# Optimization experiments

Measured on AMD Instinct MI355X. Metric: run time of the kernel, lower is better.

## Reference

```python
import jax, jax.numpy as jnp
import numpy as np

P, H, B_SZ, L = 256, 128, 4, 4096

def setup_inputs() -> dict:
    key = jax.random.key(0)
    k1, k2, k3, k4, k5 = jax.random.split(key, 5)
    A_diag = jax.random.uniform(k1, (P,), dtype=jnp.float32)                 # [P], >=0 for stability
    B = jax.random.normal(k2, (P, H, 2), dtype=jnp.float32) / np.sqrt(H)     # [P,H,2] real+imag
    C = jax.random.normal(k3, (H, P, 2), dtype=jnp.float32) / np.sqrt(P)     # [H,P,2] real+imag
    input_sequence = jax.random.normal(k4, (B_SZ, L, H), dtype=jnp.float32)  # [B,L,H]
    step = jax.random.uniform(k5, (P,), dtype=jnp.float32, minval=0.01, maxval=1.0)  # [P], 0<dt<=1
    return {"A_diag": A_diag, "B": B, "C": C, "input_sequence": input_sequence, "step": step}

def reference(A_diag, B, C, input_sequence, step):
    # LinOSS-IM: implicit discretization of a diagonal oscillatory SSM.
    cdt = jnp.complex64
    B_c = (B[..., 0] + 1j * B[..., 1]).astype(cdt)           # [P,H]
    Bu = jnp.einsum('blh,ph->blp', input_sequence.astype(cdt), B_c)  # [B,L,P]
    A_c = A_diag.astype(cdt)
    s_c = step.astype(cdt)
    schur = 1.0 / (1.0 + s_c ** 2 * A_c)                      # (I + dt^2 A)^-1, diagonal
    M11 = 1.0 - s_c ** 2 * A_c * schur
    M12 = -s_c * A_c * schur
    M21 = s_c * schur
    M22 = schur
    F1 = M11 * (s_c * Bu)                                     # [B,L,P]
    F2 = M21 * (s_c * Bu)
    Bsz = input_sequence.shape[0]
    z0 = jnp.zeros((Bsz, A_diag.shape[0]), dtype=cdt)
    y0 = jnp.zeros((Bsz, A_diag.shape[0]), dtype=cdt)

    def step_fn(carry, f):
        z, y = carry
        f1, f2 = f
        z_new = M11 * z + M12 * y + f1
        y_new = M21 * z + M22 * y + f2
        return (z_new, y_new), y_new

    # scan over time axis L; move L to front
    (z_f, y_f), ys = jax.lax.scan(step_fn, (z0, y0),
                                  (jnp.swapaxes(F1, 0, 1), jnp.swapaxes(F2, 0, 1)))
    ys = jnp.swapaxes(ys, 0, 1)                               # [B,L,P]
    C_c = (C[..., 0] + 1j * C[..., 1]).astype(cdt)            # [H,P]
    out = jnp.einsum('blp,hp->blh', ys, C_c).real.astype(jnp.float32)  # [B,L,H]
    return out, (z_f, y_f)
```

## Files before the change

### kernel.cpp

```cpp
#include <hip/hip_runtime.h>
#include <cstddef>

#define P_DIM 256
#define H_DIM 128
#define B_SZ 4
#define L_SEQ 4096
#define PC 512
#define M_ROWS (B_SZ * L_SEQ)
#define CL 32
#define CLOG 5
#define NC (L_SEQ / CL)
#define OUT_BASE (B_SZ * L_SEQ * H_DIM)

#define USE_MFMA 1

typedef __attribute__((ext_vector_type(8))) short s8v;
typedef __attribute__((ext_vector_type(4))) float f32x4;

__device__ __forceinline__ unsigned short f2bf(float x) {
  unsigned u = __builtin_bit_cast(unsigned, x);
  unsigned r = (u + 0x7FFFu + ((u >> 16) & 1u)) >> 16;
  return (unsigned short)r;
}
__device__ __forceinline__ float bf2f(unsigned short h) {
  return __builtin_bit_cast(float, (unsigned)h << 16);
}
__device__ __forceinline__ void f2hl(float x, short& h, short& l) {
  unsigned short hb = f2bf(x);
  float hf = bf2f(hb);
  unsigned short lb = f2bf(x - hf);
  h = (short)hb; l = (short)lb;
}

__device__ __forceinline__ void make_M(const float* A_diag, const float* step, int p,
                                       float& M11, float& M12, float& M21, float& M22) {
  float Ad = A_diag[p], s = step[p];
  float sig = 1.0f / fmaf(s * s, Ad, 1.0f);
  M11 = 1.0f - s * s * Ad * sig;
  M12 = -s * Ad * sig;
  M21 = s * sig;
  M22 = sig;
}

#if USE_MFMA
__global__ __launch_bounds__(256) void prep_kernel(const float* __restrict__ Bin,
                                                   const float* __restrict__ Cin,
                                                   const float* __restrict__ step,
                                                   float* __restrict__ Bw,
                                                   short* __restrict__ CtH,
                                                   short* __restrict__ CtL) {
  int idx = blockIdx.x * 256 + threadIdx.x;
  {
    int kk = idx >> 7, h = idx & 127;
    int p = kk >> 1, c = kk & 1;
    Bw[idx] = step[p] * Bin[(p * H_DIM + h) * 2 + c];
  }
  {
    int j = idx & 7, lane = (idx >> 3) & 63, ks = (idx >> 9) & 15, nt = idx >> 13;
    int h = nt * 16 + (lane & 15);
    int k = ks * 32 + (lane >> 4) * 8 + j;
    float v = Cin[(size_t)h * PC + k] * ((k & 1) ? -1.0f : 1.0f);
    short hh, ll; f2hl(v, hh, ll);
    CtH[idx] = hh; CtL[idx] = ll;
  }
}

template<int KTOT, int LDC>
__global__ __launch_bounds__(256) void gemm_nt_mfma(const float* __restrict__ A,
                                                    const float* __restrict__ Bt,
                                                    float* __restrict__ Cout) {
  __shared__ short As_h[64][72], As_l[64][72];
  __shared__ short Bs_h[128][72], Bs_l[128][72];
  const int t = threadIdx.x;
  const int lane = t & 63;
  const int wid = t >> 6;
  const int wm = (wid & 1) * 32;
  const int wn = (wid >> 1) * 64;
  const int m0 = blockIdx.y * 64;
  const int n0 = blockIdx.x * 128;
  const int lr  = lane & 15;
  const int kb8 = (lane >> 4) * 8;
  const int ar = t >> 4;
  const int ac = (t & 15) * 4;

  f32x4 acc[2][4] = {};

  for (int ks = 0; ks < KTOT / 64; ++ks) {
    const int k0 = ks * 64;
    float4 av[4], bv[8];
#pragma unroll
    for (int j = 0; j < 4; ++j)
      av[j] = *(const float4*)&A[(size_t)(m0 + ar + 16 * j) * KTOT + k0 + ac];
#pragma unroll
    for (int j = 0; j < 8; ++j)
      bv[j] = *(const float4*)&Bt[(size_t)(n0 + ar + 16 * j) * KTOT + k0 + ac];
    __syncthreads();
#pragma unroll
    for (int j = 0; j < 4; ++j) {
      short4 h4, l4;
      f2hl(av[j].x, h4.x, l4.x); f2hl(av[j].y, h4.y, l4.y);
      f2hl(av[j].z, h4.z, l4.z); f2hl(av[j].w, h4.w, l4.w);
      *(short4*)&As_h[ar + 16 * j][ac] = h4;
      *(short4*)&As_l[ar + 16 * j][ac] = l4;
    }
#pragma unroll
    for (int j = 0; j < 8; ++j) {
      short4 h4, l4;
      f2hl(bv[j].x, h4.x, l4.x); f2hl(bv[j].y, h4.y, l4.y);
      f2hl(bv[j].z, h4.z, l4.z); f2hl(bv[j].w, h4.w, l4.w);
      *(short4*)&Bs_h[ar + 16 * j][ac] = h4;
      *(short4*)&Bs_l[ar + 16 * j][ac] = l4;
    }
    __syncthreads();
#pragma unroll
    for (int kb = 0; kb < 2; ++kb) {
      s8v ah[2], al[2], bh[4], bl[4];
#pragma unroll
      for (int ti = 0; ti < 2; ++ti) {
        ah[ti] = *(const s8v*)&As_h[wm + ti * 16 + lr][kb * 32 + kb8];
        al[ti] = *(const s8v*)&As_l[wm + ti * 16 + lr][kb * 32 + kb8];
      }
#pragma unroll
      for (int tj = 0; tj < 4; ++tj) {
        bh[tj] = *(const s8v*)&Bs_h[wn + tj * 16 + lr][kb * 32 + kb8];
        bl[tj] = *(const s8v*)&Bs_l[wn + tj * 16 + lr][kb * 32 + kb8];
      }
#pragma unroll
      for (int ti = 0; ti < 2; ++ti)
#pragma unroll
        for (int tj = 0; tj < 4; ++tj) {
          acc[ti][tj] = __builtin_amdgcn_mfma_f32_16x16x32_bf16(ah[ti], bh[tj], acc[ti][tj], 0, 0, 0);
          acc[ti][tj] = __builtin_amdgcn_mfma_f32_16x16x32_bf16(ah[ti], bl[tj], acc[ti][tj], 0, 0, 0);
          acc[ti][tj] = __builtin_amdgcn_mfma_f32_16x16x32_bf16(al[ti], bh[tj], acc[ti][tj], 0, 0, 0);
        }
    }
  }
  const int rb = (lane >> 4) * 4;
#pragma unroll
  for (int ti = 0; ti < 2; ++ti)
#pragma unroll
    for (int tj = 0; tj < 4; ++tj) {
      const int row = m0 + wm + ti * 16 + rb;
      const int col = n0 + wn + tj * 16 + lr;
#pragma unroll
      for (int r = 0; r < 4; ++r)
        Cout[(size_t)(row + r) * LDC + col] = acc[ti][tj][r];
    }
}

__global__ __launch_bounds__(512) void emit_gemm_kernel(const float* __restrict__ A_diag,
                                                        const float* __restrict__ step,
                                                        const float* __restrict__ carryIn,
                                                        const float* __restrict__ sBu,
                                                        const short* __restrict__ CtH,
                                                        const short* __restrict__ CtL,
                                                        float* __restrict__ outp) {
  __shared__ short ys_h[32][512];
  __shared__ short ys_l[32][512];
  const int t = threadIdx.x;
  const int b = blockIdx.y, ch = blockIdx.x;

  {
    const int p = t >> 1;
    float M11, M12, M21, M22;
    make_M(A_diag, step, p, M11, M12, M21, M22);
    size_t o = (((size_t)b * NC + ch) * PC + t) * 2;
    float z = carryIn[o], y = carryIn[o + 1];
    const float* fp = sBu + ((size_t)b * L_SEQ + (size_t)ch * CL) * PC + t;
#pragma unroll 8
    for (int i = 0; i < CL; ++i) {
      float f = fp[(size_t)i * PC];
      float zf = z + f;
      z = fmaf(M11, zf, M12 * y);
      y = fmaf(M21, zf, M22 * y);
      short hh, ll; f2hl(y, hh, ll);
      const int c = t ^ ((i & 7) << 3);
      ys_h[i][c] = hh;
      ys_l[i][c] = ll;
    }
  }
  __syncthreads();

  const int w = t >> 6, lane = t & 63;
  const int mt = w & 1;
  const int ntb = (w >> 1) * 2;
  const int lr = lane & 15, kb8 = (lane >> 4) * 8;
  const int mrow = mt * 16 + lr;
  const int msw = (mrow & 7) << 3;
  f32x4 acc[2] = {};
  for (int ks = 0; ks < 16; ++ks) {
    const int kc = (ks * 32 + kb8) ^ msw;
    s8v ah = *(const s8v*)&ys_h[mrow][kc];
    s8v al = *(const s8v*)&ys_l[mrow][kc];
#pragma unroll
    for (int q = 0; q < 2; ++q) {
      const int nt = ntb + q;
      size_t fo = (((size_t)nt * 16 + ks) * 64 + lane) * 8;
      s8v bh = *(const s8v*)&CtH[fo];
      s8v bl = *(const s8v*)&CtL[fo];
      acc[q] = __builtin_amdgcn_mfma_f32_16x16x32_bf16(ah, bh, acc[q], 0, 0, 0);
      acc[q] = __builtin_amdgcn_mfma_f32_16x16x32_bf16(al, bh, acc[q], 0, 0, 0);
      acc[q] = __builtin_amdgcn_mfma_f32_16x16x32_bf16(ah, bl, acc[q], 0, 0, 0);
    }
  }
  const int rb = (lane >> 4) * 4;
  const size_t rowbase = (size_t)b * L_SEQ + (size_t)ch * CL;
#pragma unroll
  for (int q = 0; q < 2; ++q) {
    const int col = (ntb + q) * 16 + lr;
#pragma unroll
    for (int r = 0; r < 4; ++r) {
      int m = mt * 16 + rb + r;
      outp[(rowbase + m) * H_DIM + col] = acc[q][r];
    }
  }
}
#else
__global__ __launch_bounds__(256) void prep_kernel_f32(const float* __restrict__ Bin,
                                                       const float* __restrict__ Cin,
                                                       const float* __restrict__ step,
                                                       float* __restrict__ Bw,
                                                       float* __restrict__ Ct) {
  int idx = blockIdx.x * 256 + threadIdx.x;
  int kk = idx >> 7, h = idx & 127;
  int p = kk >> 1, c = kk & 1;
  Bw[idx] = step[p] * Bin[(p * H_DIM + h) * 2 + c];
  float cv = Cin[(h * P_DIM + p) * 2 + c];
  Ct[idx] = (c == 0) ? cv : -cv;
}

__global__ __launch_bounds__(256) void gemm_nt_kernel(const float* __restrict__ A,
                                                      const float* __restrict__ Bm,
                                                      float* __restrict__ Cout) {
  __shared__ float As[16][132];
  __shared__ float Bs[16][132];
  const int t = threadIdx.x;
  const int m0 = blockIdx.y * 128;
  const int n0 = blockIdx.x * 128;
  const int tm0 = (t & 15) * 8;
  const int tn0 = (t >> 4) * 8;
  const int row = t >> 2;
  const int kq  = (t & 3) * 4;
  float acc[8][8] = {};
  for (int k0 = 0; k0 < 128; k0 += 16) {
    float4 a0 = *(const float4*)&A[(size_t)(m0 + row) * 128 + k0 + kq];
    float4 a1 = *(const float4*)&A[(size_t)(m0 + row + 64) * 128 + k0 + kq];
    float4 b0 = *(const float4*)&Bm[(size_t)(n0 + row) * 128 + k0 + kq];
    float4 b1 = *(const float4*)&Bm[(size_t)(n0 + row + 64) * 128 + k0 + kq];
    __syncthreads();
    As[kq + 0][row] = a0.x; As[kq + 1][row] = a0.y; As[kq + 2][row] = a0.z; As[kq + 3][row] = a0.w;
    As[kq + 0][row + 64] = a1.x; As[kq + 1][row + 64] = a1.y; As[kq + 2][row + 64] = a1.z; As[kq + 3][row + 64] = a1.w;
    Bs[kq + 0][row] = b0.x; Bs[kq + 1][row] = b0.y; Bs[kq + 2][row] = b0.z; Bs[kq + 3][row] = b0.w;
    Bs[kq + 0][row + 64] = b1.x; Bs[kq + 1][row + 64] = b1.y; Bs[kq + 2][row + 64] = b1.z; Bs[kq + 3][row + 64] = b1.w;
    __syncthreads();
#pragma unroll
    for (int k = 0; k < 16; ++k) {
      float4 a03 = *(const float4*)&As[k][tm0];
      float4 a47 = *(const float4*)&As[k][tm0 + 4];
      float4 b03 = *(const float4*)&Bs[k][tn0];
      float4 b47 = *(const float4*)&Bs[k][tn0 + 4];
      float av[8] = {a03.x, a03.y, a03.z, a03.w, a47.x, a47.y, a47.z, a47.w};
      float bv[8] = {b03.x, b03.y, b03.z, b03.w, b47.x, b47.y, b47.z, b47.w};
#pragma unroll
      for (int i = 0; i < 8; ++i)
#pragma unroll
        for (int j = 0; j < 8; ++j)
          acc[i][j] = fmaf(av[i], bv[j], acc[i][j]);
    }
  }
#pragma unroll
  for (int i = 0; i < 8; ++i) {
    float4 v0 = make_float4(acc[i][0], acc[i][1], acc[i][2], acc[i][3]);
    float4 v1 = make_float4(acc[i][4], acc[i][5], acc[i][6], acc[i][7]);
    *(float4*)&Cout[(size_t)(m0 + tm0 + i) * PC + n0 + tn0] = v0;
    *(float4*)&Cout[(size_t)(m0 + tm0 + i) * PC + n0 + tn0 + 4] = v1;
  }
}

__global__ __launch_bounds__(512) void scan_emit_kernel(const float* __restrict__ A_diag,
                                                        const float* __restrict__ step,
                                                        const float* __restrict__ carryIn,
                                                        float* __restrict__ sBu) {
  const int t = threadIdx.x;
  const int p = t >> 1;
  const int b = blockIdx.y;
  const int ch = blockIdx.x;
  float M11, M12, M21, M22;
  make_M(A_diag, step, p, M11, M12, M21, M22);
  size_t o = (((size_t)b * NC + ch) * PC + t) * 2;
  float z = carryIn[o], y = carryIn[o + 1];
  float* fp = sBu + ((size_t)b * L_SEQ + (size_t)ch * CL) * PC + t;
#pragma unroll 8
  for (int i = 0; i < CL; ++i) {
    float f = fp[(size_t)i * PC];
    float zf = z + f;
    z = fmaf(M11, zf, M12 * y);
    y = fmaf(M21, zf, M22 * y);
    fp[(size_t)i * PC] = y;
  }
}

__global__ __launch_bounds__(256) void gemm_nn_kernel(const float* __restrict__ A,
                                                      const float* __restrict__ Bm,
                                                      float* __restrict__ Cout) {
  __shared__ float As[16][132];
  __shared__ float Bs[16][68];
  const int t = threadIdx.x;
  const int m0 = blockIdx.y * 128;
  const int n0 = blockIdx.x * 64;
  const int tm0 = (t & 15) * 8;
  const int tn0 = (t >> 4) * 4;
  const int row = t >> 2;
  const int kq  = (t & 3) * 4;
  const int bk_row = t >> 4;
  const int bk_c4  = (t & 15) * 4;
  float acc[8][4] = {};
  for (int k0 = 0; k0 < 512; k0 += 16) {
    float4 a0 = *(const float4*)&A[(size_t)(m0 + row) * PC + k0 + kq];
    float4 a1 = *(const float4*)&A[(size_t)(m0 + row + 64) * PC + k0 + kq];
    float4 bv = *(const float4*)&Bm[(size_t)(k0 + bk_row) * H_DIM + n0 + bk_c4];
    __syncthreads();
    As[kq + 0][row] = a0.x; As[kq + 1][row] = a0.y; As[kq + 2][row] = a0.z; As[kq + 3][row] = a0.w;
    As[kq + 0][row + 64] = a1.x; As[kq + 1][row + 64] = a1.y; As[kq + 2][row + 64] = a1.z; As[kq + 3][row + 64] = a1.w;
    *(float4*)&Bs[bk_row][bk_c4] = bv;
    __syncthreads();
#pragma unroll
    for (int k = 0; k < 16; ++k) {
      float4 a03 = *(const float4*)&As[k][tm0];
      float4 a47 = *(const float4*)&As[k][tm0 + 4];
      float4 b03 = *(const float4*)&Bs[k][tn0];
      float av[8] = {a03.x, a03.y, a03.z, a03.w, a47.x, a47.y, a47.z, a47.w};
      float bv4[4] = {b03.x, b03.y, b03.z, b03.w};
#pragma unroll
      for (int i = 0; i < 8; ++i)
#pragma unroll
        for (int j = 0; j < 4; ++j)
          acc[i][j] = fmaf(av[i], bv4[j], acc[i][j]);
    }
  }
#pragma unroll
  for (int i = 0; i < 8; ++i) {
    float4 v = make_float4(acc[i][0], acc[i][1], acc[i][2], acc[i][3]);
    *(float4*)&Cout[(size_t)(m0 + tm0 + i) * H_DIM + n0 + tn0] = v;
  }
}
#endif

__global__ __launch_bounds__(512) void scan_local_kernel(const float* __restrict__ A_diag,
                                                         const float* __restrict__ step,
                                                         const float* __restrict__ sBu,
                                                         float* __restrict__ carries) {
  const int t = threadIdx.x;
  const int p = t >> 1;
  const int b = blockIdx.y;
  const int ch = blockIdx.x;
  float M11, M12, M21, M22;
  make_M(A_diag, step, p, M11, M12, M21, M22);
  const float* fp = sBu + ((size_t)b * L_SEQ + (size_t)ch * CL) * PC + t;
  float z = 0.f, y = 0.f;
#pragma unroll 8
  for (int i = 0; i < CL; ++i) {
    float f = fp[(size_t)i * PC];
    float zf = z + f;
    z = fmaf(M11, zf, M12 * y);
    y = fmaf(M21, zf, M22 * y);
  }
  size_t o = (((size_t)b * NC + ch) * PC + t) * 2;
  carries[o] = z; carries[o + 1] = y;
}

__global__ __launch_bounds__(512) void combine_kernel(const float* __restrict__ A_diag,
                                                      const float* __restrict__ step,
                                                      const float* __restrict__ carries,
                                                      float* __restrict__ carryIn,
                                                      float* __restrict__ outp,
                                                      int mode) {
  const int t = threadIdx.x;
  const int p = t >> 1;
  const int b = blockIdx.x;
  float M11, M12, M21, M22;
  make_M(A_diag, step, p, M11, M12, M21, M22);
  float X11 = M11, X12 = M12, X21 = M21, X22 = M22;
#pragma unroll
  for (int i = 0; i < CLOG; ++i) {
    float a = X11 * X11 + X12 * X21;
    float bb = X11 * X12 + X12 * X22;
    float cc = X21 * X11 + X22 * X21;
    float dd = X21 * X12 + X22 * X22;
    X11 = a; X12 = bb; X21 = cc; X22 = dd;
  }
  float z = 0.f, y = 0.f;
#pragma unroll 4
  for (int k = 0; k < NC; ++k) {
    size_t o = (((size_t)b * NC + k) * PC + t) * 2;
    carryIn[o] = z; carryIn[o + 1] = y;
    float sz = carries[o], sy = carries[o + 1];
    float zn = X11 * z + X12 * y + sz;
    float yn = X21 * z + X22 * y + sy;
    z = zn; y = yn;
  }
  const int c = t & 1;
  if (mode == 1) {
    if (c == 0) {
      outp[OUT_BASE + (size_t)b * 256 + p] = z;
      outp[OUT_BASE + 1024 + (size_t)b * 256 + p] = y;
    }
  } else if (mode == 2) {
    outp[OUT_BASE + (size_t)c * 1024 + (size_t)b * 256 + p] = z;
    outp[OUT_BASE + 2048 + (size_t)c * 1024 + (size_t)b * 256 + p] = y;
  } else {
    outp[OUT_BASE + (size_t)b * PC + t] = z;
    outp[OUT_BASE + 2048 + (size_t)b * PC + t] = y;
  }
}

extern "C" void kernel_launch(void* const* d_in, const int* in_sizes, int n_in,
                              void* d_out, int out_size, void* d_ws, size_t ws_size,
                              hipStream_t stream) {
  const float* A_diag = (const float*)d_in[0];
  const float* Bin    = (const float*)d_in[1];
  const float* Cin    = (const float*)d_in[2];
  const float* U      = (const float*)d_in[3];
  const float* step   = (const float*)d_in[4];
  float* outp = (float*)d_out;
  float* ws = (float*)d_ws;

  int mode;
  if (out_size == OUT_BASE + 2048) mode = 1;
  else if (out_size == OUT_BASE + 4096) mode = 2;
  else mode = 0;

  float* Bw      = ws;
  float* CtA     = Bw + 65536;
  float* sBu     = CtA + 65536;
  float* carries = sBu + 8388608;
  float* carryIn = carries + 524288;

#if USE_MFMA
  short* CtH = (short*)CtA;
  short* CtL = CtH + 65536;
  prep_kernel<<<256, 256, 0, stream>>>(Bin, Cin, step, Bw, CtH, CtL);
  gemm_nt_mfma<128, 512><<<dim3(4, 256), 256, 0, stream>>>(U, Bw, sBu);
  scan_local_kernel<<<dim3(NC, B_SZ), 512, 0, stream>>>(A_diag, step, sBu, carries);
  combine_kernel<<<B_SZ, 512, 0, stream>>>(A_diag, step, carries, carryIn, outp, mode);
  emit_gemm_kernel<<<dim3(NC, B_SZ), 512, 0, stream>>>(A_diag, step, carryIn, sBu,
                                                       CtH, CtL, outp);
#else
  prep_kernel_f32<<<256, 256, 0, stream>>>(Bin, Cin, step, Bw, CtA);
  gemm_nt_kernel<<<dim3(4, 128), 256, 0, stream>>>(U, Bw, sBu);
  scan_local_kernel<<<dim3(NC, B_SZ), 512, 0, stream>>>(A_diag, step, sBu, carries);
  combine_kernel<<<B_SZ, 512, 0, stream>>>(A_diag, step, carries, carryIn, outp, mode);
  scan_emit_kernel<<<dim3(NC, B_SZ), 512, 0, stream>>>(A_diag, step, carryIn, sBu);
  gemm_nn_kernel<<<dim3(2, 128), 256, 0, stream>>>(sBu, CtA, outp);
#endif
}
```

Baseline: 126.6 us.

## Fuse input GEMM, chunk scan, combine and emit into one cooperative kernel

Replaces the separate input GEMM, local scan, carry combine and emit+output-GEMM launches with a single cooperative kernel that uses grid-wide syncs between phases. Each block computes its 32-row slice of the projected input straight into shared memory with pre-split bf16 hi/lo weights, so the large intermediate sBu buffer is never written to or read back from global memory. The combine phase now runs in only the chunk-0 blocks while every other block waits at the grid barrier. This adds grid-sync overhead and a serialized combine, and keeps the old multi-kernel path as a fallback if the cooperative launch fails.

```diff
diff --git a/kernel.cpp b/kernel.cpp
--- a/kernel.cpp
+++ b/kernel.cpp
@@ -1,18 +1,18 @@
 #include <hip/hip_runtime.h>
+#include <hip/hip_cooperative_groups.h>
 #include <cstddef>
+
+namespace cg = cooperative_groups;
 
 #define P_DIM 256
 #define H_DIM 128
 #define B_SZ 4
 #define L_SEQ 4096
 #define PC 512
-#define M_ROWS (B_SZ * L_SEQ)
 #define CL 32
 #define CLOG 5
 #define NC (L_SEQ / CL)
 #define OUT_BASE (B_SZ * L_SEQ * H_DIM)
-
-#define USE_MFMA 1
 
 typedef __attribute__((ext_vector_type(8))) short s8v;
 typedef __attribute__((ext_vector_type(4))) float f32x4;
@@ -42,13 +42,14 @@
   M22 = sig;
 }
 
-#if USE_MFMA
 __global__ __launch_bounds__(256) void prep_kernel(const float* __restrict__ Bin,
                                                    const float* __restrict__ Cin,
                                                    const float* __restrict__ step,
                                                    float* __restrict__ Bw,
                                                    short* __restrict__ CtH,
-                                                   short* __restrict__ CtL) {
+                                                   short* __restrict__ CtL,
+                                                   short* __restrict__ BwH,
+                                                   short* __restrict__ BwL) {
   int idx = blockIdx.x * 256 + threadIdx.x;
   {
     int kk = idx >> 7, h = idx & 127;
@@ -62,6 +63,188 @@
     float v = Cin[(size_t)h * PC + k] * ((k & 1) ? -1.0f : 1.0f);
     short hh, ll; f2hl(v, hh, ll);
     CtH[idx] = hh; CtL[idx] = ll;
+  }
+  {
+    int j = idx & 7, lane = (idx >> 3) & 63, ks = (idx >> 9) & 3, nt = idx >> 11;
+    int n = nt * 16 + (lane & 15);
+    int k = ks * 32 + (lane >> 4) * 8 + j;
+    int p = n >> 1, c = n & 1;
+    float v = step[p] * Bin[(p * H_DIM + k) * 2 + c];
+    short hh, ll; f2hl(v, hh, ll);
+    BwH[idx] = hh; BwL[idx] = ll;
+  }
+}
+
+__global__ __launch_bounds__(512, 4) void mega_kernel(const float* __restrict__ A_diag,
+                                                      const float* __restrict__ step,
+                                                      const float* __restrict__ U,
+                                                      const short* __restrict__ BwH,
+                                                      const short* __restrict__ BwL,
+                                                      const short* __restrict__ CtH,
+                                                      const short* __restrict__ CtL,
+                                                      float* __restrict__ carries,
+                                                      float* __restrict__ carryIn,
+                                                      float* __restrict__ outp,
+                                                      int mode) {
+  __shared__ float Fs[32][512];
+  const int t = threadIdx.x;
+  const int ch = blockIdx.x;
+  const int b  = blockIdx.y;
+  const int lane = t & 63, w = t >> 6;
+  const int lr = lane & 15, kb8 = (lane >> 4) * 8, rb = (lane >> 4) * 4;
+
+  short* Ush = (short*)&Fs[0][0];
+  short* Usl = Ush + 32 * 136;
+  {
+    const int row = t >> 4, c8 = (t & 15) * 8;
+    const float* up = &U[((size_t)b * L_SEQ + (size_t)ch * CL + row) * H_DIM + c8];
+    float4 u0 = *(const float4*)up, u1 = *(const float4*)(up + 4);
+    s8v h8, l8; short hh, ll;
+    f2hl(u0.x, hh, ll); h8[0] = hh; l8[0] = ll;
+    f2hl(u0.y, hh, ll); h8[1] = hh; l8[1] = ll;
+    f2hl(u0.z, hh, ll); h8[2] = hh; l8[2] = ll;
+    f2hl(u0.w, hh, ll); h8[3] = hh; l8[3] = ll;
+    f2hl(u1.x, hh, ll); h8[4] = hh; l8[4] = ll;
+    f2hl(u1.y, hh, ll); h8[5] = hh; l8[5] = ll;
+    f2hl(u1.z, hh, ll); h8[6] = hh; l8[6] = ll;
+    f2hl(u1.w, hh, ll); h8[7] = hh; l8[7] = ll;
+    *(s8v*)&Ush[row * 136 + c8] = h8;
+    *(s8v*)&Usl[row * 136 + c8] = l8;
+  }
+  __syncthreads();
+
+  const int mt = w & 1;
+  const int ntbA = (w >> 1) * 8;
+  f32x4 accA[8] = {};
+#pragma unroll
+  for (int ks = 0; ks < 4; ++ks) {
+    s8v ah = *(const s8v*)&Ush[(mt * 16 + lr) * 136 + ks * 32 + kb8];
+    s8v al = *(const s8v*)&Usl[(mt * 16 + lr) * 136 + ks * 32 + kb8];
+#pragma unroll
+    for (int q = 0; q < 8; ++q) {
+      size_t fo = (((size_t)(ntbA + q) * 4 + ks) * 64 + lane) * 8;
+      s8v bh = *(const s8v*)&BwH[fo];
+      s8v bl = *(const s8v*)&BwL[fo];
+      accA[q] = __builtin_amdgcn_mfma_f32_16x16x32_bf16(ah, bh, accA[q], 0, 0, 0);
+      accA[q] = __builtin_amdgcn_mfma_f32_16x16x32_bf16(al, bh, accA[q], 0, 0, 0);
+      accA[q] = __builtin_amdgcn_mfma_f32_16x16x32_bf16(ah, bl, accA[q], 0, 0, 0);
+    }
+  }
+  __syncthreads();
+
+#pragma unroll
+  for (int q = 0; q < 8; ++q)
+#pragma unroll
+    for (int r = 0; r < 4; ++r) {
+      int row = mt * 16 + rb + r;
+      int col = (ntbA + q) * 16 + lr;
+      Fs[row][col ^ ((row & 7) << 3)] = accA[q][r];
+    }
+  __syncthreads();
+
+  float M11, M12, M21, M22;
+  make_M(A_diag, step, t >> 1, M11, M12, M21, M22);
+  {
+    float z = 0.f, y = 0.f;
+#pragma unroll 8
+    for (int i = 0; i < CL; ++i) {
+      float f = Fs[i][t ^ ((i & 7) << 3)];
+      float zf = z + f;
+      z = fmaf(M11, zf, M12 * y);
+      y = fmaf(M21, zf, M22 * y);
+    }
+    size_t o = (((size_t)b * NC + ch) * PC + t) * 2;
+    carries[o] = z; carries[o + 1] = y;
+  }
+  cg::this_grid().sync();
+
+  if (ch == 0) {
+    float X11 = M11, X12 = M12, X21 = M21, X22 = M22;
+#pragma unroll
+    for (int i = 0; i < CLOG; ++i) {
+      float a = X11 * X11 + X12 * X21;
+      float bb = X11 * X12 + X12 * X22;
+      float cc = X21 * X11 + X22 * X21;
+      float dd = X21 * X12 + X22 * X22;
+      X11 = a; X12 = bb; X21 = cc; X22 = dd;
+    }
+    float z = 0.f, y = 0.f;
+#pragma unroll 8
+    for (int k = 0; k < NC; ++k) {
+      size_t o = (((size_t)b * NC + k) * PC + t) * 2;
+      carryIn[o] = z; carryIn[o + 1] = y;
+      float sz = carries[o], sy = carries[o + 1];
+      float zn = X11 * z + X12 * y + sz;
+      float yn = X21 * z + X22 * y + sy;
+      z = zn; y = yn;
+    }
+    const int c = t & 1, p = t >> 1;
+    if (mode == 1) {
+      if (c == 0) {
+        outp[OUT_BASE + (size_t)b * 256 + p] = z;
+        outp[OUT_BASE + 1024 + (size_t)b * 256 + p] = y;
+      }
+    } else if (mode == 2) {
+      outp[OUT_BASE + (size_t)c * 1024 + (size_t)b * 256 + p] = z;
+      outp[OUT_BASE + 2048 + (size_t)c * 1024 + (size_t)b * 256 + p] = y;
+    } else {
+      outp[OUT_BASE + (size_t)b * PC + t] = z;
+      outp[OUT_BASE + 2048 + (size_t)b * PC + t] = y;
+    }
+  }
+  cg::this_grid().sync();
+
+  {
+    size_t o = (((size_t)b * NC + ch) * PC + t) * 2;
+    float z = carryIn[o], y = carryIn[o + 1];
+#pragma unroll 8
+    for (int i = 0; i < CL; ++i) {
+      const int cswz = t ^ ((i & 7) << 3);
+      float f = Fs[i][cswz];
+      float zf = z + f;
+      z = fmaf(M11, zf, M12 * y);
+      y = fmaf(M21, zf, M22 * y);
+      short hh, ll; f2hl(y, hh, ll);
+      unsigned u = ((unsigned)(unsigned short)hh << 16) | (unsigned)(unsigned short)ll;
+      Fs[i][cswz] = __builtin_bit_cast(float, u);
+    }
+  }
+  __syncthreads();
+
+  const int ntbC = (w >> 1) * 2;
+  const int mrow = mt * 16 + lr;
+  const int msw = (mrow & 7) << 3;
+  f32x4 accC[2] = {};
+  for (int ks = 0; ks < 16; ++ks) {
+    const unsigned* ap = (const unsigned*)&Fs[mrow][(ks * 32 + kb8) ^ msw];
+    uint4 w0 = *(const uint4*)ap;
+    uint4 w1 = *(const uint4*)(ap + 4);
+    s8v ah, al;
+    ah[0] = (short)(w0.x >> 16); al[0] = (short)(w0.x & 0xffff);
+    ah[1] = (short)(w0.y >> 16); al[1] = (short)(w0.y & 0xffff);
+    ah[2] = (short)(w0.z >> 16); al[2] = (short)(w0.z & 0xffff);
+    ah[3] = (short)(w0.w >> 16); al[3] = (short)(w0.w & 0xffff);
+    ah[4] = (short)(w1.x >> 16); al[4] = (short)(w1.x & 0xffff);
+    ah[5] = (short)(w1.y >> 16); al[5] = (short)(w1.y & 0xffff);
+    ah[6] = (short)(w1.z >> 16); al[6] = (short)(w1.z & 0xffff);
+    ah[7] = (short)(w1.w >> 16); al[7] = (short)(w1.w & 0xffff);
+#pragma unroll
+    for (int q = 0; q < 2; ++q) {
+      size_t fo = (((size_t)(ntbC + q) * 16 + ks) * 64 + lane) * 8;
+      s8v bh = *(const s8v*)&CtH[fo];
+      s8v bl = *(const s8v*)&CtL[fo];
+      accC[q] = __builtin_amdgcn_mfma_f32_16x16x32_bf16(ah, bh, accC[q], 0, 0, 0);
+      accC[q] = __builtin_amdgcn_mfma_f32_16x16x32_bf16(al, bh, accC[q], 0, 0, 0);
+      accC[q] = __builtin_amdgcn_mfma_f32_16x16x32_bf16(ah, bl, accC[q], 0, 0, 0);
+    }
+  }
+  const size_t rowbase = (size_t)b * L_SEQ + (size_t)ch * CL;
+#pragma unroll
+  for (int q = 0; q < 2; ++q) {
+    const int col = (ntbC + q) * 16 + lr;
+#pragma unroll
+    for (int r = 0; r < 4; ++r)
+      outp[(rowbase + mt * 16 + rb + r) * H_DIM + col] = accC[q][r];
   }
 }
 
@@ -82,9 +265,7 @@
   const int kb8 = (lane >> 4) * 8;
   const int ar = t >> 4;
   const int ac = (t & 15) * 4;
-
   f32x4 acc[2][4] = {};
-
   for (int ks = 0; ks < KTOT / 64; ++ks) {
     const int k0 = ks * 64;
     float4 av[4], bv[8];
@@ -146,6 +327,71 @@
       for (int r = 0; r < 4; ++r)
         Cout[(size_t)(row + r) * LDC + col] = acc[ti][tj][r];
     }
+}
+
+__global__ __launch_bounds__(512) void scan_local_kernel(const float* __restrict__ A_diag,
+                                                         const float* __restrict__ step,
+                                                         const float* __restrict__ sBu,
+                                                         float* __restrict__ carries) {
+  const int t = threadIdx.x;
+  const int b = blockIdx.y, ch = blockIdx.x;
+  float M11, M12, M21, M22;
+  make_M(A_diag, step, t >> 1, M11, M12, M21, M22);
+  const float* fp = sBu + ((size_t)b * L_SEQ + (size_t)ch * CL) * PC + t;
+  float z = 0.f, y = 0.f;
+#pragma unroll 8
+  for (int i = 0; i < CL; ++i) {
+    float f = fp[(size_t)i * PC];
+    float zf = z + f;
+    z = fmaf(M11, zf, M12 * y);
+    y = fmaf(M21, zf, M22 * y);
+  }
+  size_t o = (((size_t)b * NC + ch) * PC + t) * 2;
+  carries[o] = z; carries[o + 1] = y;
+}
+
+__global__ __launch_bounds__(512) void combine_kernel(const float* __restrict__ A_diag,
+                                                      const float* __restrict__ step,
+                                                      const float* __restrict__ carries,
+                                                      float* __restrict__ carryIn,
+                                                      float* __restrict__ outp,
+                                                      int mode) {
+  const int t = threadIdx.x;
+  const int b = blockIdx.x;
+  float M11, M12, M21, M22;
+  make_M(A_diag, step, t >> 1, M11, M12, M21, M22);
+  float X11 = M11, X12 = M12, X21 = M21, X22 = M22;
+#pragma unroll
+  for (int i = 0; i < CLOG; ++i) {
+    float a = X11 * X11 + X12 * X21;
+    float bb = X11 * X12 + X12 * X22;
+    float cc = X21 * X11 + X22 * X21;
+    float dd = X21 * X12 + X22 * X22;
+    X11 = a; X12 = bb; X21 = cc; X22 = dd;
+  }
+  float z = 0.f, y = 0.f;
+#pragma unroll 8
+  for (int k = 0; k < NC; ++k) {
+    size_t o = (((size_t)b * NC + k) * PC + t) * 2;
+    carryIn[o] = z; carryIn[o + 1] = y;
+    float sz = carries[o], sy = carries[o + 1];
+    float zn = X11 * z + X12 * y + sz;
+    float yn = X21 * z + X22 * y + sy;
+    z = zn; y = yn;
+  }
+  const int c = t & 1, p = t >> 1;
+  if (mode == 1) {
+    if (c == 0) {
+      outp[OUT_BASE + (size_t)b * 256 + p] = z;
+      outp[OUT_BASE + 1024 + (size_t)b * 256 + p] = y;
+    }
+  } else if (mode == 2) {
+    outp[OUT_BASE + (size_t)c * 1024 + (size_t)b * 256 + p] = z;
+    outp[OUT_BASE + 2048 + (size_t)c * 1024 + (size_t)b * 256 + p] = y;
+  } else {
+    outp[OUT_BASE + (size_t)b * PC + t] = z;
+    outp[OUT_BASE + 2048 + (size_t)b * PC + t] = y;
+  }
 }
 
 __global__ __launch_bounds__(512) void emit_gemm_kernel(const float* __restrict__ A_diag,
@@ -159,11 +405,9 @@
   __shared__ short ys_l[32][512];
   const int t = threadIdx.x;
   const int b = blockIdx.y, ch = blockIdx.x;
-
-  {
-    const int p = t >> 1;
+  {
     float M11, M12, M21, M22;
-    make_M(A_diag, step, p, M11, M12, M21, M22);
+    make_M(A_diag, step, t >> 1, M11, M12, M21, M22);
     size_t o = (((size_t)b * NC + ch) * PC + t) * 2;
     float z = carryIn[o], y = carryIn[o + 1];
     const float* fp = sBu + ((size_t)b * L_SEQ + (size_t)ch * CL) * PC + t;
@@ -180,7 +424,6 @@
     }
   }
   __syncthreads();
-
   const int w = t >> 6, lane = t & 63;
   const int mt = w & 1;
   const int ntb = (w >> 1) * 2;
@@ -194,8 +437,7 @@
     s8v al = *(const s8v*)&ys_l[mrow][kc];
 #pragma unroll
     for (int q = 0; q < 2; ++q) {
-      const int nt = ntb + q;
-      size_t fo = (((size_t)nt * 16 + ks) * 64 + lane) * 8;
+      size_t fo = (((size_t)(ntb + q) * 16 + ks) * 64 + lane) * 8;
       s8v bh = *(const s8v*)&CtH[fo];
       s8v bl = *(const s8v*)&CtL[fo];
       acc[q] = __builtin_amdgcn_mfma_f32_16x16x32_bf16(ah, bh, acc[q], 0, 0, 0);
@@ -209,208 +451,8 @@
   for (int q = 0; q < 2; ++q) {
     const int col = (ntb + q) * 16 + lr;
 #pragma unroll
-    for (int r = 0; r < 4; ++r) {
-      int m = mt * 16 + rb + r;
-      outp[(rowbase + m) * H_DIM + col] = acc[q][r];
-    }
-  }
-}
-#else
-__global__ __launch_bounds__(256) void prep_kernel_f32(const float* __restrict__ Bin,
-                                                       const float* __restrict__ Cin,
-                                                       const float* __restrict__ step,
-                                                       float* __restrict__ Bw,
-                                                       float* __restrict__ Ct) {
-  int idx = blockIdx.x * 256 + threadIdx.x;
-  int kk = idx >> 7, h = idx & 127;
-  int p = kk >> 1, c = kk & 1;
-  Bw[idx] = step[p] * Bin[(p * H_DIM + h) * 2 + c];
-  float cv = Cin[(h * P_DIM + p) * 2 + c];
-  Ct[idx] = (c == 0) ? cv : -cv;
-}
-
-__global__ __launch_bounds__(256) void gemm_nt_kernel(const float* __restrict__ A,
-                                                      const float* __restrict__ Bm,
-                                                      float* __restrict__ Cout) {
-  __shared__ float As[16][132];
-  __shared__ float Bs[16][132];
-  const int t = threadIdx.x;
-  const int m0 = blockIdx.y * 128;
-  const int n0 = blockIdx.x * 128;
-  const int tm0 = (t & 15) * 8;
-  const int tn0 = (t >> 4) * 8;
-  const int row = t >> 2;
-  const int kq  = (t & 3) * 4;
-  float acc[8][8] = {};
-  for (int k0 = 0; k0 < 128; k0 += 16) {
-    float4 a0 = *(const float4*)&A[(size_t)(m0 + row) * 128 + k0 + kq];
-    float4 a1 = *(const float4*)&A[(size_t)(m0 + row + 64) * 128 + k0 + kq];
-    float4 b0 = *(const float4*)&Bm[(size_t)(n0 + row) * 128 + k0 + kq];
-    float4 b1 = *(const float4*)&Bm[(size_t)(n0 + row + 64) * 128 + k0 + kq];
-    __syncthreads();
-    As[kq + 0][row] = a0.x; As[kq + 1][row] = a0.y; As[kq + 2][row] = a0.z; As[kq + 3][row] = a0.w;
-    As[kq + 0][row + 64] = a1.x; As[kq + 1][row + 64] = a1.y; As[kq + 2][row + 64] = a1.z; As[kq + 3][row + 64] = a1.w;
-    Bs[kq + 0][row] = b0.x; Bs[kq + 1][row] = b0.y; Bs[kq + 2][row] = b0.z; Bs[kq + 3][row] = b0.w;
-    Bs[kq + 0][row + 64] = b1.x; Bs[kq + 1][row + 64] = b1.y; Bs[kq + 2][row + 64] = b1.z; Bs[kq + 3][row + 64] = b1.w;
-    __syncthreads();
-#pragma unroll
-    for (int k = 0; k < 16; ++k) {
-      float4 a03 = *(const float4*)&As[k][tm0];
-      float4 a47 = *(const float4*)&As[k][tm0 + 4];
-      float4 b03 = *(const float4*)&Bs[k][tn0];
-      float4 b47 = *(const float4*)&Bs[k][tn0 + 4];
-      float av[8] = {a03.x, a03.y, a03.z, a03.w, a47.x, a47.y, a47.z, a47.w};
-      float bv[8] = {b03.x, b03.y, b03.z, b03.w, b47.x, b47.y, b47.z, b47.w};
-#pragma unroll
-      for (int i = 0; i < 8; ++i)
-#pragma unroll
-        for (int j = 0; j < 8; ++j)
-          acc[i][j] = fmaf(av[i], bv[j], acc[i][j]);
-    }
-  }
-#pragma unroll
-  for (int i = 0; i < 8; ++i) {
-    float4 v0 = make_float4(acc[i][0], acc[i][1], acc[i][2], acc[i][3]);
-    float4 v1 = make_float4(acc[i][4], acc[i][5], acc[i][6], acc[i][7]);
-    *(float4*)&Cout[(size_t)(m0 + tm0 + i) * PC + n0 + tn0] = v0;
-    *(float4*)&Cout[(size_t)(m0 + tm0 + i) * PC + n0 + tn0 + 4] = v1;
-  }
-}
-
-__global__ __launch_bounds__(512) void scan_emit_kernel(const float* __restrict__ A_diag,
-                                                        const float* __restrict__ step,
-                                                        const float* __restrict__ carryIn,
-                                                        float* __restrict__ sBu) {
-  const int t = threadIdx.x;
-  const int p = t >> 1;
-  const int b = blockIdx.y;
-  const int ch = blockIdx.x;
-  float M11, M12, M21, M22;
-  make_M(A_diag, step, p, M11, M12, M21, M22);
-  size_t o = (((size_t)b * NC + ch) * PC + t) * 2;
-  float z = carryIn[o], y = carryIn[o + 1];
-  float* fp = sBu + ((size_t)b * L_SEQ + (size_t)ch * CL) * PC + t;
-#pragma unroll 8
-  for (int i = 0; i < CL; ++i) {
-    float f = fp[(size_t)i * PC];
-    float zf = z + f;
-    z = fmaf(M11, zf, M12 * y);
-    y = fmaf(M21, zf, M22 * y);
-    fp[(size_t)i * PC] = y;
-  }
-}
-
-__global__ __launch_bounds__(256) void gemm_nn_kernel(const float* __restrict__ A,
-                                                      const float* __restrict__ Bm,
-                                                      float* __restrict__ Cout) {
-  __shared__ float As[16][132];
-  __shared__ float Bs[16][68];
-  const int t = threadIdx.x;
-  const int m0 = blockIdx.y * 128;
-  const int n0 = blockIdx.x * 64;
-  const int tm0 = (t & 15) * 8;
-  const int tn0 = (t >> 4) * 4;
-  const int row = t >> 2;
-  const int kq  = (t & 3) * 4;
-  const int bk_row = t >> 4;
-  const int bk_c4  = (t & 15) * 4;
-  float acc[8][4] = {};
-  for (int k0 = 0; k0 < 512; k0 += 16) {
-    float4 a0 = *(const float4*)&A[(size_t)(m0 + row) * PC + k0 + kq];
-    float4 a1 = *(const float4*)&A[(size_t)(m0 + row + 64) * PC + k0 + kq];
-    float4 bv = *(const float4*)&Bm[(size_t)(k0 + bk_row) * H_DIM + n0 + bk_c4];
-    __syncthreads();
-    As[kq + 0][row] = a0.x; As[kq + 1][row] = a0.y; As[kq + 2][row] = a0.z; As[kq + 3][row] = a0.w;
-    As[kq + 0][row + 64] = a1.x; As[kq + 1][row + 64] = a1.y; As[kq + 2][row + 64] = a1.z; As[kq + 3][row + 64] = a1.w;
-    *(float4*)&Bs[bk_row][bk_c4] = bv;
-    __syncthreads();
-#pragma unroll
-    for (int k = 0; k < 16; ++k) {
-      float4 a03 = *(const float4*)&As[k][tm0];
-      float4 a47 = *(const float4*)&As[k][tm0 + 4];
-      float4 b03 = *(const float4*)&Bs[k][tn0];
-      float av[8] = {a03.x, a03.y, a03.z, a03.w, a47.x, a47.y, a47.z, a47.w};
-      float bv4[4] = {b03.x, b03.y, b03.z, b03.w};
-#pragma unroll
-      for (int i = 0; i < 8; ++i)
-#pragma unroll
-        for (int j = 0; j < 4; ++j)
-          acc[i][j] = fmaf(av[i], bv4[j], acc[i][j]);
-    }
-  }
-#pragma unroll
-  for (int i = 0; i < 8; ++i) {
-    float4 v = make_float4(acc[i][0], acc[i][1], acc[i][2], acc[i][3]);
-    *(float4*)&Cout[(size_t)(m0 + tm0 + i) * H_DIM + n0 + tn0] = v;
-  }
-}
-#endif
-
-__global__ __launch_bounds__(512) void scan_local_kernel(const float* __restrict__ A_diag,
-                                                         const float* __restrict__ step,
-                                                         const float* __restrict__ sBu,
-                                                         float* __restrict__ carries) {
-  const int t = threadIdx.x;
-  const int p = t >> 1;
-  const int b = blockIdx.y;
-  const int ch = blockIdx.x;
-  float M11, M12, M21, M22;
-  make_M(A_diag, step, p, M11, M12, M21, M22);
-  const float* fp = sBu + ((size_t)b * L_SEQ + (size_t)ch * CL) * PC + t;
-  float z = 0.f, y = 0.f;
-#pragma unroll 8
-  for (int i = 0; i < CL; ++i) {
-    float f = fp[(size_t)i * PC];
-    float zf = z + f;
-    z = fmaf(M11, zf, M12 * y);
-    y = fmaf(M21, zf, M22 * y);
-  }
-  size_t o = (((size_t)b * NC + ch) * PC + t) * 2;
-  carries[o] = z; carries[o + 1] = y;
-}
-
-__global__ __launch_bounds__(512) void combine_kernel(const float* __restrict__ A_diag,
-                                                      const float* __restrict__ step,
-                                                      const float* __restrict__ carries,
-                                                      float* __restrict__ carryIn,
-                                                      float* __restrict__ outp,
-                                                      int mode) {
-  const int t = threadIdx.x;
-  const int p = t >> 1;
-  const int b = blockIdx.x;
-  float M11, M12, M21, M22;
-  make_M(A_diag, step, p, M11, M12, M21, M22);
-  float X11 = M11, X12 = M12, X21 = M21, X22 = M22;
-#pragma unroll
-  for (int i = 0; i < CLOG; ++i) {
-    float a = X11 * X11 + X12 * X21;
-    float bb = X11 * X12 + X12 * X22;
-    float cc = X21 * X11 + X22 * X21;
-    float dd = X21 * X12 + X22 * X22;
-    X11 = a; X12 = bb; X21 = cc; X22 = dd;
-  }
-  float z = 0.f, y = 0.f;
-#pragma unroll 4
-  for (int k = 0; k < NC; ++k) {
-    size_t o = (((size_t)b * NC + k) * PC + t) * 2;
-    carryIn[o] = z; carryIn[o + 1] = y;
-    float sz = carries[o], sy = carries[o + 1];
-    float zn = X11 * z + X12 * y + sz;
-    float yn = X21 * z + X22 * y + sy;
-    z = zn; y = yn;
-  }
-  const int c = t & 1;
-  if (mode == 1) {
-    if (c == 0) {
-      outp[OUT_BASE + (size_t)b * 256 + p] = z;
-      outp[OUT_BASE + 1024 + (size_t)b * 256 + p] = y;
-    }
-  } else if (mode == 2) {
-    outp[OUT_BASE + (size_t)c * 1024 + (size_t)b * 256 + p] = z;
-    outp[OUT_BASE + 2048 + (size_t)c * 1024 + (size_t)b * 256 + p] = y;
-  } else {
-    outp[OUT_BASE + (size_t)b * PC + t] = z;
-    outp[OUT_BASE + 2048 + (size_t)b * PC + t] = y;
+    for (int r = 0; r < 4; ++r)
+      outp[(rowbase + mt * 16 + rb + r) * H_DIM + col] = acc[q][r];
   }
 }
 
@@ -431,26 +473,27 @@
   else mode = 0;
 
   float* Bw      = ws;
-  float* CtA     = Bw + 65536;
-  float* sBu     = CtA + 65536;
-  float* carries = sBu + 8388608;
-  float* carryIn = carries + 524288;
-
-#if USE_MFMA
-  short* CtH = (short*)CtA;
-  short* CtL = CtH + 65536;
-  prep_kernel<<<256, 256, 0, stream>>>(Bin, Cin, step, Bw, CtH, CtL);
-  gemm_nt_mfma<128, 512><<<dim3(4, 256), 256, 0, stream>>>(U, Bw, sBu);
-  scan_local_kernel<<<dim3(NC, B_SZ), 512, 0, stream>>>(A_diag, step, sBu, carries);
-  combine_kernel<<<B_SZ, 512, 0, stream>>>(A_diag, step, carries, carryIn, outp, mode);
-  emit_gemm_kernel<<<dim3(NC, B_SZ), 512, 0, stream>>>(A_diag, step, carryIn, sBu,
-                                                       CtH, CtL, outp);
-#else
-  prep_kernel_f32<<<256, 256, 0, stream>>>(Bin, Cin, step, Bw, CtA);
-  gemm_nt_kernel<<<dim3(4, 128), 256, 0, stream>>>(U, Bw, sBu);
-  scan_local_kernel<<<dim3(NC, B_SZ), 512, 0, stream>>>(A_diag, step, sBu, carries);
-  combine_kernel<<<B_SZ, 512, 0, stream>>>(A_diag, step, carries, carryIn, outp, mode);
-  scan_emit_kernel<<<dim3(NC, B_SZ), 512, 0, stream>>>(A_diag, step, carryIn, sBu);
-  gemm_nn_kernel<<<dim3(2, 128), 256, 0, stream>>>(sBu, CtA, outp);
-#endif
-}
+  short* CtH     = (short*)(ws + 65536);
+  short* CtL     = CtH + 65536;
+  short* BwH     = (short*)(ws + 131072);
+  short* BwL     = BwH + 65536;
+  float* carries = ws + 196608;
+  float* carryIn = ws + 720896;
+  float* sBu     = ws + 1245184;
+
+  prep_kernel<<<256, 256, 0, stream>>>(Bin, Cin, step, Bw, CtH, CtL, BwH, BwL);
+
+  void* args[] = {(void*)&A_diag, (void*)&step, (void*)&U,
+                  (void*)&BwH, (void*)&BwL, (void*)&CtH, (void*)&CtL,
+                  (void*)&carries, (void*)&carryIn, (void*)&outp, (void*)&mode};
+  hipError_t e = hipLaunchCooperativeKernel((void*)mega_kernel,
+                                            dim3(NC, B_SZ), dim3(512),
+                                            args, 0, stream);
+  if (e != hipSuccess) {
+    gemm_nt_mfma<128, 512><<<dim3(4, 256), 256, 0, stream>>>(U, Bw, sBu);
+    scan_local_kernel<<<dim3(NC, B_SZ), 512, 0, stream>>>(A_diag, step, sBu, carries);
+    combine_kernel<<<B_SZ, 512, 0, stream>>>(A_diag, step, carries, carryIn, outp, mode);
+    emit_gemm_kernel<<<dim3(NC, B_SZ), 512, 0, stream>>>(A_diag, step, carryIn, sBu,
+                                                         CtH, CtL, outp);
+  }
+}
```

Result: slower. 234.7 us (+85.4%).
